# Kernel optimization log

Measured on AMD Instinct MI355X. Metric: run time of the kernel, lower is better.

## Reference

```python
import jax, jax.numpy as jnp
import numpy as np

B, I, J, N, C, H = 1, 256, 64, 384, 256, 8
CH = C // H  # per-head channels
EPS = 1e-5


def layer_norm(x, scale, bias):
    mu = jnp.mean(x, axis=-1, keepdims=True)
    var = jnp.mean(jnp.square(x - mu), axis=-1, keepdims=True)
    return (x - mu) * jax.lax.rsqrt(var + EPS) * scale + bias


def setup_inputs() -> dict:
    key = jax.random.key(0)
    ks = jax.random.split(key, 12)
    s = 0.02
    return {
        "rigids_embed": jax.random.normal(ks[0], (B, I, N, C), dtype=jnp.float32),
        "rigids_memory": jax.random.normal(ks[1], (J, N, C), dtype=jnp.float32),
        "rigids_mask": jax.random.randint(ks[2], (B, I, N), 0, 2, dtype=jnp.int32),
        "memory_mask": jax.random.randint(ks[3], (J, N), 0, 2, dtype=jnp.int32),
        "ln_q_scale": jnp.ones((C,), jnp.float32),
        "ln_q_bias": jnp.zeros((C,), jnp.float32),
        "ln_kv_scale": jnp.ones((C,), jnp.float32),
        "ln_kv_bias": jnp.zeros((C,), jnp.float32),
        "Wq": jax.random.normal(ks[4], (C, C), dtype=jnp.float32) * s,
        "Wkv": jax.random.normal(ks[5], (C, 2 * C), dtype=jnp.float32) * s,
        "Wgate": jax.random.normal(ks[6], (C, C), dtype=jnp.float32) * s,
        "Wout": jax.random.normal(ks[7], (C, C), dtype=jnp.float32) * s,
        "ln_ffn_scale": jnp.ones((C,), jnp.float32),
        "ln_ffn_bias": jnp.zeros((C,), jnp.float32),
        "W1": jax.random.normal(ks[8], (C, 2 * C), dtype=jnp.float32) * s,
        "b1": jnp.zeros((2 * C,), jnp.float32),
        "W2": jax.random.normal(ks[9], (2 * C, C), dtype=jnp.float32) * s,
        "b2": jnp.zeros((C,), jnp.float32),
    }


def reference(rigids_embed, rigids_memory, rigids_mask, memory_mask,
              ln_q_scale, ln_q_bias, ln_kv_scale, ln_kv_bias,
              Wq, Wkv, Wgate, Wout,
              ln_ffn_scale, ln_ffn_bias, W1, b1, W2, b2):
    rmask = rigids_mask.astype(jnp.float32)   # [B,I,N]
    mmask = memory_mask.astype(jnp.float32)   # [J,N]

    # ---- gated cross-attention ----
    qe = layer_norm(rigids_embed, ln_q_scale, ln_q_bias)      # [B,I,N,C]
    km = layer_norm(rigids_memory, ln_kv_scale, ln_kv_bias)   # [J,N,C]

    # mask: [B,I,1,N] * [1,1,J,N] -> [B,I,J,N]
    mask = rmask[:, :, None, :] * mmask[None, None]

    q = (qe @ Wq).reshape(B, I, N, H, CH)                      # [B,I,N,H,CH]
    kv = (km @ Wkv).reshape(J, N, 2 * H, CH)                   # [J,N,2H,CH]
    k, v = kv[:, :, :H, :], kv[:, :, H:, :]                    # [J,N,H,CH] each

    a = jnp.einsum('binhc,jnhc->bijnh', q, k)                  # [B,I,J,N,H]
    a = a + (mask[..., None] - 1.0) * 1e6
    a = jax.nn.softmax(a, axis=-1)  # NOTE: softmax over heads, as in source

    out = jnp.einsum('bijnh,jnhc->binhc', a, v)                # [B,I,N,H,CH]
    gate = (qe @ Wgate).reshape(out.shape)
    out = out * jax.nn.sigmoid(gate)
    out = out.reshape(B, I, N, C) @ Wout
    out = out * rmask[..., None]

    x = rigids_embed + out

    # ---- Transition FFN (LN -> Linear(C,2C) -> ReLU -> Linear(2C,C)) ----
    h = layer_norm(x, ln_ffn_scale, ln_ffn_bias)
    h = jax.nn.relu(h @ W1 + b1) @ W2 + b2
    x = x + h * rmask[..., None]
    return x
```

## Files before the change

kernel.cpp:

```cpp
#include <hip/hip_runtime.h>
#include <math.h>

using u16 = unsigned short;
using u32 = unsigned int;

typedef __attribute__((ext_vector_type(4))) float f32x4;
typedef __attribute__((ext_vector_type(8))) short s16x8;

__device__ __forceinline__ u16 f2bf(float f) {
  union { float f; u32 u; } c; c.f = f;
  u32 u = c.u;
  u += 0x7fffu + ((u >> 16) & 1u);
  return (u16)(u >> 16);
}
__device__ __forceinline__ float bf2f(u16 s) {
  union { u32 u; float f; } c; c.u = ((u32)s) << 16;
  return c.f;
}
__device__ __forceinline__ void async16(const void* g, void* l) {
  __builtin_amdgcn_global_load_lds(
      (const __attribute__((address_space(1))) void*)g,
      (__attribute__((address_space(3))) void*)l, 16, 0, 0);
}

__global__ __launch_bounds__(256) void ln_kernel(
    const float* __restrict__ x, const float* __restrict__ sc,
    const float* __restrict__ bi, u16* __restrict__ out) {
  const int w = threadIdx.x >> 6, l = threadIdx.x & 63;
  const int row = blockIdx.x * 4 + w;
  const float4 v = ((const float4*)(x + (size_t)row * 256))[l];
  float s  = v.x + v.y + v.z + v.w;
  float s2 = v.x * v.x + v.y * v.y + v.z * v.z + v.w * v.w;
#pragma unroll
  for (int m = 1; m < 64; m <<= 1) {
    s  += __shfl_xor(s,  m, 64);
    s2 += __shfl_xor(s2, m, 64);
  }
  const float mean = s * (1.0f / 256.0f);
  const float var  = s2 * (1.0f / 256.0f) - mean * mean;
  const float rs   = rsqrtf(var + 1e-5f);
  const float4 s4 = ((const float4*)sc)[l];
  const float4 b4 = ((const float4*)bi)[l];
  u16 o0 = f2bf((v.x - mean) * rs * s4.x + b4.x);
  u16 o1 = f2bf((v.y - mean) * rs * s4.y + b4.y);
  u16 o2 = f2bf((v.z - mean) * rs * s4.z + b4.z);
  u16 o3 = f2bf((v.w - mean) * rs * s4.w + b4.w);
  uint2 p; p.x = (u32)o0 | ((u32)o1 << 16); p.y = (u32)o2 | ((u32)o3 << 16);
  *(uint2*)(out + (size_t)row * 256 + l * 4) = p;
}

__global__ __launch_bounds__(256) void convw_kernel(
    const float* s0, const float* s1, const float* s2, const float* s3,
    const float* s4, const float* s5,
    u16* d0, u16* d1, u16* d2, u16* d3, u16* d4, u16* d5) {
  const float* s; u16* d; int K, N, sh;
  switch (blockIdx.y) {
    case 0: s = s0; d = d0; K = 256; N = 256; sh = 8; break;
    case 1: s = s1; d = d1; K = 256; N = 256; sh = 8; break;
    case 2: s = s2; d = d2; K = 256; N = 512; sh = 9; break;
    case 3: s = s3; d = d3; K = 256; N = 256; sh = 8; break;
    case 4: s = s4; d = d4; K = 256; N = 512; sh = 9; break;
    default: s = s5; d = d5; K = 512; N = 256; sh = 8; break;
  }
  const int idx = blockIdx.x * 256 + threadIdx.x;
  if (idx >= K * N) return;
  const int k = idx >> sh, n = idx & (N - 1);
  d[(size_t)n * K + k] = f2bf(s[idx]);
}

__global__ __launch_bounds__(256) void vtrans_kernel(const u16* __restrict__ KV,
                                                     u16* __restrict__ VT) {
  const int n = blockIdx.x, h = blockIdx.y;
  const int t = threadIdx.x;
  const int j = t >> 2, cg = t & 3;
  union { uint4 v; u16 u[8]; } d;
  d.v = *(const uint4*)(KV + ((size_t)(j * 384 + n)) * 512 + 256 + h * 32 + cg * 8);
  u16* dst = VT + (((size_t)n * 8 + h) * 32 + cg * 8) * 64 + j;
#pragma unroll
  for (int c = 0; c < 8; c++) dst[c * 64] = d.u[c];
}

__global__ __launch_bounds__(256) void gemm_kernel(
    const u16* __restrict__ A, const u16* __restrict__ BT,
    const int K, const int N,
    u16* __restrict__ outb, float* __restrict__ outf,
    const float* __restrict__ bias, const float* __restrict__ res,
    const int* __restrict__ rmask, const int epi) {
  __shared__ u16 Als[128 * 32];
  __shared__ u16 Bls[128 * 32];
  const int t = threadIdx.x, w = t >> 6, l = t & 63;
  const int mb = blockIdx.y * 128, nb = blockIdx.x * 128;
  const int lm = l & 15, lk = l >> 4;

  const int cg = (l & 3) ^ ((l >> 3) & 3);
  const int rA = w * 32 + (l >> 2);
  const u16* gA = A  + (size_t)(mb + rA) * K + cg * 8;
  const u16* gB = BT + (size_t)(nb + rA) * K + cg * 8;
  u16* lA0 = &Als[(w * 32) * 32];
  u16* lA1 = &Als[(w * 32 + 16) * 32];
  u16* lB0 = &Bls[(w * 32) * 32];
  u16* lB1 = &Bls[(w * 32 + 16) * 32];
  const size_t rk16 = (size_t)16 * K;

  const int pc = (lk ^ ((l >> 1) & 3)) * 8;
  const int m0 = (w >> 1) * 64, n0 = (w & 1) * 64;

  f32x4 acc[4][4] = {};

  for (int kk = 0; kk < K; kk += 32) {
    if (kk) __syncthreads();
    async16(gA + kk, lA0);
    async16(gA + rk16 + kk, lA1);
    async16(gB + kk, lB0);
    async16(gB + rk16 + kk, lB1);
    __syncthreads();
    s16x8 a[4], b[4];
#pragma unroll
    for (int i = 0; i < 4; i++) a[i] = *(const s16x8*)&Als[(m0 + i * 16 + lm) * 32 + pc];
#pragma unroll
    for (int j = 0; j < 4; j++) b[j] = *(const s16x8*)&Bls[(n0 + j * 16 + lm) * 32 + pc];
#pragma unroll
    for (int i = 0; i < 4; i++)
#pragma unroll
      for (int j = 0; j < 4; j++)
        acc[i][j] = __builtin_amdgcn_mfma_f32_16x16x32_bf16(a[i], b[j], acc[i][j], 0, 0, 0);
  }

  const int r0 = mb + m0 + lk * 4;
  const int c0 = nb + n0 + lm;
  if (epi == 0) {
#pragma unroll
    for (int i = 0; i < 4; i++)
#pragma unroll
      for (int j = 0; j < 4; j++)
#pragma unroll
        for (int r = 0; r < 4; r++)
          outb[(size_t)(r0 + i * 16 + r) * N + (c0 + j * 16)] = f2bf(acc[i][j][r]);
  } else if (epi == 1) {
#pragma unroll
    for (int i = 0; i < 4; i++)
#pragma unroll
      for (int j = 0; j < 4; j++)
#pragma unroll
        for (int r = 0; r < 4; r++) {
          const int col = c0 + j * 16;
          const float v = fmaxf(acc[i][j][r] + bias[col], 0.0f);
          outb[(size_t)(r0 + i * 16 + r) * N + col] = f2bf(v);
        }
  } else if (epi == 2) {
#pragma unroll
    for (int i = 0; i < 4; i++)
#pragma unroll
      for (int r = 0; r < 4; r++) {
        const int row = r0 + i * 16 + r;
        const float rm = (float)rmask[row];
#pragma unroll
        for (int j = 0; j < 4; j++) {
          const size_t idx = (size_t)row * N + (c0 + j * 16);
          outf[idx] = res[idx] + acc[i][j][r] * rm;
        }
      }
  } else {
#pragma unroll
    for (int i = 0; i < 4; i++)
#pragma unroll
      for (int r = 0; r < 4; r++) {
        const int row = r0 + i * 16 + r;
        const float rm = (float)rmask[row];
#pragma unroll
        for (int j = 0; j < 4; j++) {
          const int col = c0 + j * 16;
          const size_t idx = (size_t)row * N + col;
          outf[idx] = outf[idx] + (acc[i][j][r] + bias[col]) * rm;
        }
      }
  }
}

__global__ __launch_bounds__(256) void attn_kernel(
    const u16* __restrict__ QG, const u16* __restrict__ KV,
    const u16* __restrict__ VT, u16* __restrict__ O) {
  __shared__ u16 P[8][16][72];
  const int n = blockIdx.x, ig = blockIdx.y;
  const int t = threadIdx.x, w = t >> 6, l = t & 63;
  const int lm = l & 15, lk = l >> 4;

  const u16* qb = QG + ((size_t)(ig * 16 + lm) * 384 + n) * 512 + lk * 8;
  const u16* kb = KV + ((size_t)(w * 16 + lm) * 384 + n) * 512 + lk * 8;
  const f32x4 zz = {0.f, 0.f, 0.f, 0.f};
  f32x4 acc[8];
#pragma unroll
  for (int h = 0; h < 8; h++) {
    s16x8 af = *(const s16x8*)(qb + h * 32);
    s16x8 bf = *(const s16x8*)(kb + h * 32);
    acc[h] = __builtin_amdgcn_mfma_f32_16x16x32_bf16(af, bf, zz, 0, 0, 0);
  }
#pragma unroll
  for (int r = 0; r < 4; r++) {
    float mx = acc[0][r];
#pragma unroll
    for (int h = 1; h < 8; h++) mx = fmaxf(mx, acc[h][r]);
    float e[8], s = 0.f;
#pragma unroll
    for (int h = 0; h < 8; h++) { e[h] = __expf(acc[h][r] - mx); s += e[h]; }
    const float inv = 1.0f / s;
#pragma unroll
    for (int h = 0; h < 8; h++) P[h][lk * 4 + r][w * 16 + lm] = f2bf(e[h] * inv);
  }
  __syncthreads();

  const u16* vb = VT + ((size_t)n * 8) * 2048;
#pragma unroll
  for (int hh = 0; hh < 2; hh++) {
    const int h = w * 2 + hh;
#pragma unroll
    for (int nt = 0; nt < 2; nt++) {
      f32x4 o = zz;
#pragma unroll
      for (int ks = 0; ks < 2; ks++) {
        s16x8 af = *(const s16x8*)&P[h][lm][ks * 32 + lk * 8];
        s16x8 bf = *(const s16x8*)(vb + (size_t)h * 2048 + (nt * 16 + lm) * 64 + ks * 32 + lk * 8);
        o = __builtin_amdgcn_mfma_f32_16x16x32_bf16(af, bf, o, 0, 0, 0);
      }
#pragma unroll
      for (int r = 0; r < 4; r++) {
        const int i = ig * 16 + lk * 4 + r;
        const int col = h * 32 + nt * 16 + lm;
        const size_t orow = (size_t)i * 384 + n;
        const float g = bf2f(QG[orow * 512 + 256 + col]);
        const float val = o[r] / (1.0f + __expf(-g));
        O[orow * 256 + col] = f2bf(val);
      }
    }
  }
}

extern "C" void kernel_launch(void* const* d_in, const int* in_sizes, int n_in,
                              void* d_out, int out_size, void* d_ws, size_t ws_size,
                              hipStream_t stream) {
  (void)in_sizes; (void)n_in; (void)out_size; (void)ws_size;
  const float* embed  = (const float*)d_in[0];
  const float* memory = (const float*)d_in[1];
  const int*   rmask  = (const int*)d_in[2];
  const float* lnqs = (const float*)d_in[4];
  const float* lnqb = (const float*)d_in[5];
  const float* lnks = (const float*)d_in[6];
  const float* lnkb = (const float*)d_in[7];
  const float* Wq   = (const float*)d_in[8];
  const float* Wkv  = (const float*)d_in[9];
  const float* Wg   = (const float*)d_in[10];
  const float* Wo   = (const float*)d_in[11];
  const float* lnfs = (const float*)d_in[12];
  const float* lnfb = (const float*)d_in[13];
  const float* W1   = (const float*)d_in[14];
  const float* b1   = (const float*)d_in[15];
  const float* W2   = (const float*)d_in[16];
  const float* b2   = (const float*)d_in[17];
  float* out = (float*)d_out;
  char* ws = (char*)d_ws;

  u16* qe   = (u16*)(ws + 0);
  u16* km   = (u16*)(ws + 50331648);
  u16* VT   = km;
  u16* QG   = (u16*)(ws + 62914560);
  u16* h1   = QG;
  u16* KV   = (u16*)(ws + 163577856);
  u16* O    = (u16*)(ws + 188743680);
  u16* WQGT = (u16*)(ws + 239075328);
  u16* WKVT = WQGT + 131072;
  u16* WOUTT= WKVT + 131072;
  u16* W1T  = WOUTT + 65536;
  u16* W2T  = W1T + 131072;
  u16* lnx  = qe;

  convw_kernel<<<dim3(512, 6), 256, 0, stream>>>(Wq, Wg, Wkv, Wo, W1, W2,
      WQGT, WQGT + 65536, WKVT, WOUTT, W1T, W2T);
  ln_kernel<<<24576, 256, 0, stream>>>(embed, lnqs, lnqb, qe);
  ln_kernel<<<6144, 256, 0, stream>>>(memory, lnks, lnkb, km);
  gemm_kernel<<<dim3(4, 768), 256, 0, stream>>>(qe, WQGT, 256, 512, QG, nullptr, nullptr, nullptr, nullptr, 0);
  gemm_kernel<<<dim3(4, 192), 256, 0, stream>>>(km, WKVT, 256, 512, KV, nullptr, nullptr, nullptr, nullptr, 0);
  vtrans_kernel<<<dim3(384, 8), 256, 0, stream>>>(KV, VT);
  attn_kernel<<<dim3(384, 16), 256, 0, stream>>>(QG, KV, VT, O);
  gemm_kernel<<<dim3(2, 768), 256, 0, stream>>>(O, WOUTT, 256, 256, nullptr, out, nullptr, embed, rmask, 2);
  ln_kernel<<<24576, 256, 0, stream>>>(out, lnfs, lnfb, lnx);
  gemm_kernel<<<dim3(4, 768), 256, 0, stream>>>(lnx, W1T, 256, 512, h1, nullptr, b1, nullptr, nullptr, 1);
  gemm_kernel<<<dim3(2, 768), 256, 0, stream>>>(h1, W2T, 512, 256, nullptr, out, b2, nullptr, rmask, 3);
}
```

Measured before the change: 654.4 us.

## Fuse FFN GEMMs into one kernel and load GEMM operands directly from global

The two FFN GEMMs are fused into one kernel. Each 128-row tile computes its W1 hidden chunk, applies bias and ReLU, stores it in swizzled LDS as bf16, and multiplies it by W2 right away. This removes the h1 round trip through global memory and one launch. The general GEMM also drops its LDS staging and instead loads MFMA fragments straight from global memory into registers, double-buffered and specialised to K=256. In exchange, with two column blocks per row tile, each block recomputes the whole first GEMM, doubling its work. Removing LDS reuse also raises global and L2 traffic.

```diff
diff --git a/kernel.cpp b/kernel.cpp
--- a/kernel.cpp
+++ b/kernel.cpp
@@ -16,11 +16,6 @@
 __device__ __forceinline__ float bf2f(u16 s) {
   union { u32 u; float f; } c; c.u = ((u32)s) << 16;
   return c.f;
-}
-__device__ __forceinline__ void async16(const void* g, void* l) {
-  __builtin_amdgcn_global_load_lds(
-      (const __attribute__((address_space(1))) void*)g,
-      (__attribute__((address_space(3))) void*)l, 16, 0, 0);
 }
 
 __global__ __launch_bounds__(256) void ln_kernel(
@@ -80,50 +75,40 @@
   for (int c = 0; c < 8; c++) dst[c * 64] = d.u[c];
 }
 
-__global__ __launch_bounds__(256) void gemm_kernel(
-    const u16* __restrict__ A, const u16* __restrict__ BT,
-    const int K, const int N,
+__global__ __launch_bounds__(256) void gemm256(
+    const u16* __restrict__ A, const u16* __restrict__ BT, const int N,
     u16* __restrict__ outb, float* __restrict__ outf,
-    const float* __restrict__ bias, const float* __restrict__ res,
-    const int* __restrict__ rmask, const int epi) {
-  __shared__ u16 Als[128 * 32];
-  __shared__ u16 Bls[128 * 32];
+    const float* __restrict__ res, const int* __restrict__ rmask, const int epi) {
   const int t = threadIdx.x, w = t >> 6, l = t & 63;
+  const int lm = l & 15, lk = l >> 4;
   const int mb = blockIdx.y * 128, nb = blockIdx.x * 128;
-  const int lm = l & 15, lk = l >> 4;
-
-  const int cg = (l & 3) ^ ((l >> 3) & 3);
-  const int rA = w * 32 + (l >> 2);
-  const u16* gA = A  + (size_t)(mb + rA) * K + cg * 8;
-  const u16* gB = BT + (size_t)(nb + rA) * K + cg * 8;
-  u16* lA0 = &Als[(w * 32) * 32];
-  u16* lA1 = &Als[(w * 32 + 16) * 32];
-  u16* lB0 = &Bls[(w * 32) * 32];
-  u16* lB1 = &Bls[(w * 32 + 16) * 32];
-  const size_t rk16 = (size_t)16 * K;
-
-  const int pc = (lk ^ ((l >> 1) & 3)) * 8;
   const int m0 = (w >> 1) * 64, n0 = (w & 1) * 64;
 
+  const u16* aP = A  + (size_t)(mb + m0 + lm) * 256 + lk * 8;
+  const u16* bP = BT + (size_t)(nb + n0 + lm) * 256 + lk * 8;
+
   f32x4 acc[4][4] = {};
-
-  for (int kk = 0; kk < K; kk += 32) {
-    if (kk) __syncthreads();
-    async16(gA + kk, lA0);
-    async16(gA + rk16 + kk, lA1);
-    async16(gB + kk, lB0);
-    async16(gB + rk16 + kk, lB1);
-    __syncthreads();
-    s16x8 a[4], b[4];
-#pragma unroll
-    for (int i = 0; i < 4; i++) a[i] = *(const s16x8*)&Als[(m0 + i * 16 + lm) * 32 + pc];
-#pragma unroll
-    for (int j = 0; j < 4; j++) b[j] = *(const s16x8*)&Bls[(n0 + j * 16 + lm) * 32 + pc];
+  s16x8 a[2][4], b[2][4];
+#pragma unroll
+  for (int i = 0; i < 4; i++) {
+    a[0][i] = *(const s16x8*)(aP + i * 16 * 256);
+    b[0][i] = *(const s16x8*)(bP + i * 16 * 256);
+  }
+#pragma unroll
+  for (int kc = 0; kc < 8; kc++) {
+    const int cur = kc & 1, nxt = cur ^ 1;
+    if (kc < 7) {
+#pragma unroll
+      for (int i = 0; i < 4; i++) {
+        a[nxt][i] = *(const s16x8*)(aP + i * 16 * 256 + (kc + 1) * 32);
+        b[nxt][i] = *(const s16x8*)(bP + i * 16 * 256 + (kc + 1) * 32);
+      }
+    }
 #pragma unroll
     for (int i = 0; i < 4; i++)
 #pragma unroll
       for (int j = 0; j < 4; j++)
-        acc[i][j] = __builtin_amdgcn_mfma_f32_16x16x32_bf16(a[i], b[j], acc[i][j], 0, 0, 0);
+        acc[i][j] = __builtin_amdgcn_mfma_f32_16x16x32_bf16(a[cur][i], b[cur][j], acc[i][j], 0, 0, 0);
   }
 
   const int r0 = mb + m0 + lk * 4;
@@ -136,18 +121,7 @@
 #pragma unroll
         for (int r = 0; r < 4; r++)
           outb[(size_t)(r0 + i * 16 + r) * N + (c0 + j * 16)] = f2bf(acc[i][j][r]);
-  } else if (epi == 1) {
-#pragma unroll
-    for (int i = 0; i < 4; i++)
-#pragma unroll
-      for (int j = 0; j < 4; j++)
-#pragma unroll
-        for (int r = 0; r < 4; r++) {
-          const int col = c0 + j * 16;
-          const float v = fmaxf(acc[i][j][r] + bias[col], 0.0f);
-          outb[(size_t)(r0 + i * 16 + r) * N + col] = f2bf(v);
-        }
-  } else if (epi == 2) {
+  } else {
 #pragma unroll
     for (int i = 0; i < 4; i++)
 #pragma unroll
@@ -160,21 +134,95 @@
           outf[idx] = res[idx] + acc[i][j][r] * rm;
         }
       }
-  } else {
+  }
+}
+
+__global__ __launch_bounds__(256) void ffn_kernel(
+    const u16* __restrict__ lnx, const u16* __restrict__ W1T,
+    const u16* __restrict__ W2T, const float* __restrict__ b1,
+    const float* __restrict__ b2, const float* __restrict__ x,
+    const int* __restrict__ rmask, float* __restrict__ out) {
+  __shared__ u16 hbuf[4 * 128 * 32];
+  const int t = threadIdx.x, w = t >> 6, l = t & 63;
+  const int lm = l & 15, lk = l >> 4;
+  const int rb = blockIdx.y * 128, cb = blockIdx.x * 128;
+  const int m0 = (w >> 1) * 64, n0 = (w & 1) * 64;
+
+  const u16* aP = lnx + (size_t)(rb + m0 + lm) * 256 + lk * 8;
+
+  f32x4 acc[4][4] = {};
+  const f32x4 zz = {0.f, 0.f, 0.f, 0.f};
+
+  for (int nc = 0; nc < 4; nc++) {
+    f32x4 ah[4][4];
 #pragma unroll
     for (int i = 0; i < 4; i++)
 #pragma unroll
-      for (int r = 0; r < 4; r++) {
-        const int row = r0 + i * 16 + r;
-        const float rm = (float)rmask[row];
-#pragma unroll
-        for (int j = 0; j < 4; j++) {
-          const int col = c0 + j * 16;
-          const size_t idx = (size_t)row * N + col;
-          outf[idx] = outf[idx] + (acc[i][j][r] + bias[col]) * rm;
+      for (int j = 0; j < 4; j++) ah[i][j] = zz;
+    const u16* b1P = W1T + (size_t)(nc * 128 + n0 + lm) * 256 + lk * 8;
+#pragma unroll
+    for (int kc = 0; kc < 8; kc++) {
+      s16x8 a[4], b[4];
+#pragma unroll
+      for (int i = 0; i < 4; i++) {
+        a[i] = *(const s16x8*)(aP + i * 16 * 256 + kc * 32);
+        b[i] = *(const s16x8*)(b1P + i * 16 * 256 + kc * 32);
+      }
+#pragma unroll
+      for (int i = 0; i < 4; i++)
+#pragma unroll
+        for (int j = 0; j < 4; j++)
+          ah[i][j] = __builtin_amdgcn_mfma_f32_16x16x32_bf16(a[i], b[j], ah[i][j], 0, 0, 0);
+    }
+    if (nc) __syncthreads();
+#pragma unroll
+    for (int j = 0; j < 4; j++) {
+      const int c = n0 + j * 16 + lm;
+      const float bv = b1[nc * 128 + c];
+      const int kc2 = c >> 5, lc = (c >> 3) & 3, c7 = c & 7;
+#pragma unroll
+      for (int i = 0; i < 4; i++)
+#pragma unroll
+        for (int r = 0; r < 4; r++) {
+          const int row = m0 + i * 16 + lk * 4 + r;
+          const float v = fmaxf(ah[i][j][r] + bv, 0.0f);
+          hbuf[kc2 * 4096 + row * 32 + ((lc ^ ((row >> 1) & 3)) << 3) + c7] = f2bf(v);
         }
-      }
-  }
+    }
+    __syncthreads();
+    const u16* b2P = W2T + (size_t)(cb + n0 + lm) * 512 + nc * 128 + lk * 8;
+#pragma unroll
+    for (int kc = 0; kc < 4; kc++) {
+      s16x8 a[4], b[4];
+#pragma unroll
+      for (int i = 0; i < 4; i++) {
+        const int row = m0 + i * 16 + lm;
+        a[i] = *(const s16x8*)&hbuf[kc * 4096 + row * 32 + ((lk ^ ((row >> 1) & 3)) << 3)];
+        b[i] = *(const s16x8*)(b2P + i * 16 * 512 + kc * 32);
+      }
+#pragma unroll
+      for (int i = 0; i < 4; i++)
+#pragma unroll
+        for (int j = 0; j < 4; j++)
+          acc[i][j] = __builtin_amdgcn_mfma_f32_16x16x32_bf16(a[i], b[j], acc[i][j], 0, 0, 0);
+    }
+  }
+
+  const int r0 = rb + m0 + lk * 4;
+  const int c0 = cb + n0 + lm;
+#pragma unroll
+  for (int i = 0; i < 4; i++)
+#pragma unroll
+    for (int r = 0; r < 4; r++) {
+      const int row = r0 + i * 16 + r;
+      const float rm = (float)rmask[row];
+#pragma unroll
+      for (int j = 0; j < 4; j++) {
+        const int col = c0 + j * 16;
+        const size_t idx = (size_t)row * 256 + col;
+        out[idx] = x[idx] + (acc[i][j][r] + b2[col]) * rm;
+      }
+    }
 }
 
 __global__ __launch_bounds__(256) void attn_kernel(
@@ -263,7 +311,6 @@
   u16* km   = (u16*)(ws + 50331648);
   u16* VT   = km;
   u16* QG   = (u16*)(ws + 62914560);
-  u16* h1   = QG;
   u16* KV   = (u16*)(ws + 163577856);
   u16* O    = (u16*)(ws + 188743680);
   u16* WQGT = (u16*)(ws + 239075328);
@@ -277,12 +324,11 @@
       WQGT, WQGT + 65536, WKVT, WOUTT, W1T, W2T);
   ln_kernel<<<24576, 256, 0, stream>>>(embed, lnqs, lnqb, qe);
   ln_kernel<<<6144, 256, 0, stream>>>(memory, lnks, lnkb, km);
-  gemm_kernel<<<dim3(4, 768), 256, 0, stream>>>(qe, WQGT, 256, 512, QG, nullptr, nullptr, nullptr, nullptr, 0);
-  gemm_kernel<<<dim3(4, 192), 256, 0, stream>>>(km, WKVT, 256, 512, KV, nullptr, nullptr, nullptr, nullptr, 0);
+  gemm256<<<dim3(4, 768), 256, 0, stream>>>(qe, WQGT, 512, QG, nullptr, nullptr, nullptr, 0);
+  gemm256<<<dim3(4, 192), 256, 0, stream>>>(km, WKVT, 512, KV, nullptr, nullptr, nullptr, 0);
   vtrans_kernel<<<dim3(384, 8), 256, 0, stream>>>(KV, VT);
   attn_kernel<<<dim3(384, 16), 256, 0, stream>>>(QG, KV, VT, O);
-  gemm_kernel<<<dim3(2, 768), 256, 0, stream>>>(O, WOUTT, 256, 256, nullptr, out, nullptr, embed, rmask, 2);
+  gemm256<<<dim3(2, 768), 256, 0, stream>>>(O, WOUTT, 256, nullptr, out, embed, rmask, 2);
   ln_kernel<<<24576, 256, 0, stream>>>(out, lnfs, lnfb, lnx);
-  gemm_kernel<<<dim3(4, 768), 256, 0, stream>>>(lnx, W1T, 256, 512, h1, nullptr, b1, nullptr, nullptr, 1);
-  gemm_kernel<<<dim3(2, 768), 256, 0, stream>>>(h1, W2T, 512, 256, nullptr, out, b2, nullptr, rmask, 3);
-}
+  ffn_kernel<<<dim3(2, 768), 256, 0, stream>>>(lnx, W1T, W2T, b1, b2, out, rmask, out);
+}
```

New measurement: 766.8 us. 1.17x slower.

## Register-prefetch GEMM tiles two steps ahead and stage attention gate/output through LDS

Applied to the files above, without the earlier changes.

The GEMM replaces direct global-to-LDS async loads with register prefetch. Tiles for the next two K-steps are held in registers and written to LDS between barriers, so global latency overlaps with MFMA work. In the attention kernel, gate values are loaded coalesced into LDS and the gated output is staged in LDS, then written out with 16-byte row stores instead of scattered 2-byte accesses. This adds registers, LDS use and extra barriers, which may lower occupancy.

```diff
diff --git a/kernel.cpp b/kernel.cpp
--- a/kernel.cpp
+++ b/kernel.cpp
@@ -17,11 +17,9 @@
   union { u32 u; float f; } c; c.u = ((u32)s) << 16;
   return c.f;
 }
-__device__ __forceinline__ void async16(const void* g, void* l) {
-  __builtin_amdgcn_global_load_lds(
-      (const __attribute__((address_space(1))) void*)g,
-      (__attribute__((address_space(3))) void*)l, 16, 0, 0);
-}
+
+#define BAR() do { asm volatile("s_waitcnt lgkmcnt(0)" ::: "memory"); \
+                   __builtin_amdgcn_s_barrier(); } while (0)
 
 __global__ __launch_bounds__(256) void ln_kernel(
     const float* __restrict__ x, const float* __restrict__ sc,
@@ -80,7 +78,7 @@
   for (int c = 0; c < 8; c++) dst[c * 64] = d.u[c];
 }
 
-__global__ __launch_bounds__(256) void gemm_kernel(
+__global__ __launch_bounds__(256) void gemm_v3(
     const u16* __restrict__ A, const u16* __restrict__ BT,
     const int K, const int N,
     u16* __restrict__ outb, float* __restrict__ outf,
@@ -89,41 +87,78 @@
   __shared__ u16 Als[128 * 32];
   __shared__ u16 Bls[128 * 32];
   const int t = threadIdx.x, w = t >> 6, l = t & 63;
+  const int lm = l & 15, lk = l >> 4;
   const int mb = blockIdx.y * 128, nb = blockIdx.x * 128;
-  const int lm = l & 15, lk = l >> 4;
-
-  const int cg = (l & 3) ^ ((l >> 3) & 3);
-  const int rA = w * 32 + (l >> 2);
-  const u16* gA = A  + (size_t)(mb + rA) * K + cg * 8;
-  const u16* gB = BT + (size_t)(nb + rA) * K + cg * 8;
-  u16* lA0 = &Als[(w * 32) * 32];
-  u16* lA1 = &Als[(w * 32 + 16) * 32];
-  u16* lB0 = &Bls[(w * 32) * 32];
-  u16* lB1 = &Bls[(w * 32 + 16) * 32];
+  const int m0 = (w >> 1) * 64, n0 = (w & 1) * 64;
+
+  const int srow = l >> 2;
+  const int scg  = (l & 3) ^ ((srow >> 1) & 3);
+  const u16* gA = A  + (size_t)(mb + w * 32 + srow) * K + scg * 8;
+  const u16* gB = BT + (size_t)(nb + w * 32 + srow) * K + scg * 8;
   const size_t rk16 = (size_t)16 * K;
-
-  const int pc = (lk ^ ((l >> 1) & 3)) * 8;
-  const int m0 = (w >> 1) * 64, n0 = (w & 1) * 64;
-
+  u16* wA0 = &Als[w * 1024 + l * 8];
+  u16* wA1 = wA0 + 16 * 32;
+  u16* wB0 = &Bls[w * 1024 + l * 8];
+  u16* wB1 = wB0 + 16 * 32;
+
+  const int pc = (lk ^ ((lm >> 1) & 3)) * 8;
   f32x4 acc[4][4] = {};
 
-  for (int kk = 0; kk < K; kk += 32) {
-    if (kk) __syncthreads();
-    async16(gA + kk, lA0);
-    async16(gA + rk16 + kk, lA1);
-    async16(gB + kk, lB0);
-    async16(gB + rk16 + kk, lB1);
-    __syncthreads();
-    s16x8 a[4], b[4];
-#pragma unroll
-    for (int i = 0; i < 4; i++) a[i] = *(const s16x8*)&Als[(m0 + i * 16 + lm) * 32 + pc];
-#pragma unroll
-    for (int j = 0; j < 4; j++) b[j] = *(const s16x8*)&Bls[(n0 + j * 16 + lm) * 32 + pc];
-#pragma unroll
-    for (int i = 0; i < 4; i++)
-#pragma unroll
-      for (int j = 0; j < 4; j++)
-        acc[i][j] = __builtin_amdgcn_mfma_f32_16x16x32_bf16(a[i], b[j], acc[i][j], 0, 0, 0);
+  uint4 a00 = *(const uint4*)gA;
+  uint4 a01 = *(const uint4*)(gA + rk16);
+  uint4 b00 = *(const uint4*)gB;
+  uint4 b01 = *(const uint4*)(gB + rk16);
+  uint4 a10 = *(const uint4*)(gA + 32);
+  uint4 a11 = *(const uint4*)(gA + rk16 + 32);
+  uint4 b10 = *(const uint4*)(gB + 32);
+  uint4 b11 = *(const uint4*)(gB + rk16 + 32);
+
+  const int NI = K >> 5;
+  for (int it = 0; it < NI; it += 2) {
+    *(uint4*)wA0 = a00; *(uint4*)wA1 = a01;
+    *(uint4*)wB0 = b00; *(uint4*)wB1 = b01;
+    BAR();
+    if (it + 2 < NI) {
+      a00 = *(const uint4*)(gA + (it + 2) * 32);
+      a01 = *(const uint4*)(gA + rk16 + (it + 2) * 32);
+      b00 = *(const uint4*)(gB + (it + 2) * 32);
+      b01 = *(const uint4*)(gB + rk16 + (it + 2) * 32);
+    }
+    {
+      s16x8 af[4], bf[4];
+#pragma unroll
+      for (int i = 0; i < 4; i++) af[i] = *(const s16x8*)&Als[(m0 + i * 16 + lm) * 32 + pc];
+#pragma unroll
+      for (int j = 0; j < 4; j++) bf[j] = *(const s16x8*)&Bls[(n0 + j * 16 + lm) * 32 + pc];
+#pragma unroll
+      for (int i = 0; i < 4; i++)
+#pragma unroll
+        for (int j = 0; j < 4; j++)
+          acc[i][j] = __builtin_amdgcn_mfma_f32_16x16x32_bf16(af[i], bf[j], acc[i][j], 0, 0, 0);
+    }
+    BAR();
+    *(uint4*)wA0 = a10; *(uint4*)wA1 = a11;
+    *(uint4*)wB0 = b10; *(uint4*)wB1 = b11;
+    BAR();
+    if (it + 3 < NI) {
+      a10 = *(const uint4*)(gA + (it + 3) * 32);
+      a11 = *(const uint4*)(gA + rk16 + (it + 3) * 32);
+      b10 = *(const uint4*)(gB + (it + 3) * 32);
+      b11 = *(const uint4*)(gB + rk16 + (it + 3) * 32);
+    }
+    {
+      s16x8 af[4], bf[4];
+#pragma unroll
+      for (int i = 0; i < 4; i++) af[i] = *(const s16x8*)&Als[(m0 + i * 16 + lm) * 32 + pc];
+#pragma unroll
+      for (int j = 0; j < 4; j++) bf[j] = *(const s16x8*)&Bls[(n0 + j * 16 + lm) * 32 + pc];
+#pragma unroll
+      for (int i = 0; i < 4; i++)
+#pragma unroll
+        for (int j = 0; j < 4; j++)
+          acc[i][j] = __builtin_amdgcn_mfma_f32_16x16x32_bf16(af[i], bf[j], acc[i][j], 0, 0, 0);
+    }
+    BAR();
   }
 
   const int r0 = mb + m0 + lk * 4;
@@ -181,9 +216,19 @@
     const u16* __restrict__ QG, const u16* __restrict__ KV,
     const u16* __restrict__ VT, u16* __restrict__ O) {
   __shared__ u16 P[8][16][72];
+  __shared__ u16 Gld[16][264];
+  __shared__ u16 Old[16][264];
   const int n = blockIdx.x, ig = blockIdx.y;
   const int t = threadIdx.x, w = t >> 6, l = t & 63;
   const int lm = l & 15, lk = l >> 4;
+
+#pragma unroll
+  for (int itg = 0; itg < 2; itg++) {
+    const int idx = itg * 256 + t;
+    const int r = idx >> 5, ch = idx & 31;
+    uint4 g = *(const uint4*)(QG + ((size_t)(ig * 16 + r) * 384 + n) * 512 + 256 + ch * 8);
+    *(uint4*)&Gld[r][ch * 8] = g;
+  }
 
   const u16* qb = QG + ((size_t)(ig * 16 + lm) * 384 + n) * 512 + lk * 8;
   const u16* kb = KV + ((size_t)(w * 16 + lm) * 384 + n) * 512 + lk * 8;
@@ -224,14 +269,20 @@
       }
 #pragma unroll
       for (int r = 0; r < 4; r++) {
-        const int i = ig * 16 + lk * 4 + r;
+        const int row = lk * 4 + r;
         const int col = h * 32 + nt * 16 + lm;
-        const size_t orow = (size_t)i * 384 + n;
-        const float g = bf2f(QG[orow * 512 + 256 + col]);
-        const float val = o[r] / (1.0f + __expf(-g));
-        O[orow * 256 + col] = f2bf(val);
+        const float g = bf2f(Gld[row][col]);
+        Old[row][col] = f2bf(o[r] / (1.0f + __expf(-g)));
       }
     }
+  }
+  __syncthreads();
+#pragma unroll
+  for (int itg = 0; itg < 2; itg++) {
+    const int idx = itg * 256 + t;
+    const int r = idx >> 5, ch = idx & 31;
+    uint4 val = *(const uint4*)&Old[r][ch * 8];
+    *(uint4*)(O + ((size_t)(ig * 16 + r) * 384 + n) * 256 + ch * 8) = val;
   }
 }
 
@@ -277,12 +328,12 @@
       WQGT, WQGT + 65536, WKVT, WOUTT, W1T, W2T);
   ln_kernel<<<24576, 256, 0, stream>>>(embed, lnqs, lnqb, qe);
   ln_kernel<<<6144, 256, 0, stream>>>(memory, lnks, lnkb, km);
-  gemm_kernel<<<dim3(4, 768), 256, 0, stream>>>(qe, WQGT, 256, 512, QG, nullptr, nullptr, nullptr, nullptr, 0);
-  gemm_kernel<<<dim3(4, 192), 256, 0, stream>>>(km, WKVT, 256, 512, KV, nullptr, nullptr, nullptr, nullptr, 0);
+  gemm_v3<<<dim3(4, 768), 256, 0, stream>>>(qe, WQGT, 256, 512, QG, nullptr, nullptr, nullptr, nullptr, 0);
+  gemm_v3<<<dim3(4, 192), 256, 0, stream>>>(km, WKVT, 256, 512, KV, nullptr, nullptr, nullptr, nullptr, 0);
   vtrans_kernel<<<dim3(384, 8), 256, 0, stream>>>(KV, VT);
   attn_kernel<<<dim3(384, 16), 256, 0, stream>>>(QG, KV, VT, O);
-  gemm_kernel<<<dim3(2, 768), 256, 0, stream>>>(O, WOUTT, 256, 256, nullptr, out, nullptr, embed, rmask, 2);
+  gemm_v3<<<dim3(2, 768), 256, 0, stream>>>(O, WOUTT, 256, 256, nullptr, out, nullptr, embed, rmask, 2);
   ln_kernel<<<24576, 256, 0, stream>>>(out, lnfs, lnfb, lnx);
-  gemm_kernel<<<dim3(4, 768), 256, 0, stream>>>(lnx, W1T, 256, 512, h1, nullptr, b1, nullptr, nullptr, 1);
-  gemm_kernel<<<dim3(2, 768), 256, 0, stream>>>(h1, W2T, 512, 256, nullptr, out, b2, nullptr, rmask, 3);
-}
+  gemm_v3<<<dim3(4, 768), 256, 0, stream>>>(lnx, W1T, 256, 512, h1, nullptr, b1, nullptr, nullptr, 1);
+  gemm_v3<<<dim3(2, 768), 256, 0, stream>>>(h1, W2T, 512, 256, nullptr, out, b2, nullptr, rmask, 3);
+}
```

Result: slower. 667.7 us (+2.0%).
